# Kernel optimization log

Hardware: AMD Instinct MI355X
Metric: run time of the kernel (lower is better)

The kernel has to match this reference:

```python
import jax, jax.numpy as jnp
import numpy as np

EPS = 1e-7

def squash(t, axis=-1):
    sq = jnp.sum(jnp.square(t), axis=axis, keepdims=True)
    safe_norm = jnp.sqrt(sq + EPS)
    return t * (sq / (1.0 + sq)) / safe_norm


def setup_inputs() -> dict:
    key = jax.random.key(0)
    k1, k2 = jax.random.split(key)
    B, I, Din, N, D = 32, 1024, 32, 64, 32
    x = jax.random.normal(k1, (B, I, Din), dtype=jnp.float32)
    # glorot-ish scale ~ sqrt(2/(Din+D)) = 0.1767; use 0.1
    W = jax.random.normal(k2, (N, I, D, Din), dtype=jnp.float32) * 0.1
    return {"x": x, "W": W, "num_routing": 3}


def _infer(inputs_hat, logits):
    # softmax over the num_capsule axis (axis=1), matching tf.nn.softmax(logits, axis=1)
    route = jax.nn.softmax(logits, axis=1)                      # [B,N,1,I]
    routing = jnp.squeeze(jnp.matmul(route, inputs_hat), -2)    # [B,N,D]
    return squash(routing)


def reference(x, W, num_routing):
    # inputs_hat[b,n,i,d] = sum_k x[b,i,k] * W[n,i,d,k]
    inputs_hat = jnp.einsum('bik,nidk->bnid', x, W)             # [B,N,I,D]
    B, N, I, D = inputs_hat.shape
    ih_stop = jax.lax.stop_gradient(inputs_hat)
    logits = jnp.zeros((B, N, 1, I), dtype=inputs_hat.dtype)
    outputs = None
    for r in range(num_routing):
        if r == num_routing - 1:
            outputs = _infer(inputs_hat, logits)
        else:
            outputs = _infer(ih_stop, logits)
            # distances[b,n,1,i] = <outputs[b,n,:], ih_stop[b,n,i,:]>
            dist = jnp.matmul(outputs[:, :, None, :], jnp.swapaxes(ih_stop, -1, -2))
            logits = logits + dist
    return outputs
```

## Files before the change

### kernel.cpp

```cpp
#include <hip/hip_runtime.h>
#include <stdint.h>

#define II 1024
#define BBc 32
#define NN 64
#define DD 32
#define NDT 2048

typedef _Float16 half8 __attribute__((ext_vector_type(8)));
typedef float f32x4 __attribute__((ext_vector_type(4)));

__device__ __forceinline__ half8 ld_cvt8(const float* __restrict__ p) {
  const float4 v0 = *(const float4*)p;
  const float4 v1 = *(const float4*)(p + 4);
  half8 h;
  h[0] = (_Float16)v0.x; h[1] = (_Float16)v0.y; h[2] = (_Float16)v0.z; h[3] = (_Float16)v0.w;
  h[4] = (_Float16)v1.x; h[5] = (_Float16)v1.y; h[6] = (_Float16)v1.z; h[7] = (_Float16)v1.w;
  return h;
}

__global__ __launch_bounds__(256) void k1_mfma(
    const float* __restrict__ x, const float* __restrict__ W,
    _Float16* __restrict__ ih)
{
  __shared__ _Float16 lbuf[4][32][64];
  const int t = threadIdx.x;
  const int i = blockIdx.x;
  const int half_ = blockIdx.y;
  const int w = t >> 6;
  const int L = t & 63;
  const int lm = L & 15, q = L >> 4;

  half8 afrag[2];
#pragma unroll
  for (int mt = 0; mt < 2; ++mt)
    afrag[mt] = ld_cvt8(x + ((size_t)(mt * 16 + lm) * II + i) * 32 + q * 8);

  const int ndw = half_ * 1024 + w * 256;
  for (int g = 0; g < 4; ++g) {
#pragma unroll
    for (int nt = 0; nt < 4; ++nt) {
      const int nd = ndw + g * 64 + nt * 16 + lm;
      const int n = nd >> 5, d = nd & 31;
      const half8 bfrag = ld_cvt8(W + (size_t)n * (II * 1024) + (size_t)i * 1024 + d * 32 + q * 8);
      const f32x4 z = {0.f, 0.f, 0.f, 0.f};
      f32x4 acc0 = __builtin_amdgcn_mfma_f32_16x16x32_f16(afrag[0], bfrag, z, 0, 0, 0);
      f32x4 acc1 = __builtin_amdgcn_mfma_f32_16x16x32_f16(afrag[1], bfrag, z, 0, 0, 0);
#pragma unroll
      for (int r = 0; r < 4; ++r) {
        lbuf[w][q * 4 + r][nt * 16 + lm]      = (_Float16)acc0[r];
        lbuf[w][16 + q * 4 + r][nt * 16 + lm] = (_Float16)acc1[r];
      }
    }
    __syncthreads();
#pragma unroll
    for (int j = 0; j < 4; ++j) {
      const int row = j * 8 + (L >> 3);
      const int ndo = (L & 7) * 8;
      const half8 v = *(const half8*)&lbuf[w][row][ndo];
      *(half8*)(ih + ((size_t)row * II + i) * NDT + ndw + g * 64 + ndo) = v;
    }
    __syncthreads();
  }
}

__global__ __launch_bounds__(256) void s0red(
    const _Float16* __restrict__ ih, float* __restrict__ s0p)
{
  const int b = blockIdx.x, is = blockIdx.y;
  const int t = threadIdx.x;
  const _Float16* base = ih + ((size_t)b * II + is * 64) * NDT + t * 8;
  float a[8] = {};
#pragma unroll 8
  for (int ii = 0; ii < 64; ++ii) {
    const half8 v = *(const half8*)(base + (size_t)ii * NDT);
#pragma unroll
    for (int j = 0; j < 8; ++j) a[j] += (float)v[j];
  }
  float* o = s0p + ((size_t)is * BBc + b) * NDT + t * 8;
  *(float4*)(o + 0) = make_float4(a[0], a[1], a[2], a[3]);
  *(float4*)(o + 4) = make_float4(a[4], a[5], a[6], a[7]);
}

__global__ __launch_bounds__(256) void k3_route(
    const _Float16* __restrict__ ih, const float* __restrict__ o1,
    const float* __restrict__ o2, float* __restrict__ rpart)
{
  __shared__ float red[4][NN][DD + 1];
  const int t = threadIdx.x;
  const int b = blockIdx.x, it = blockIdx.y;
  const int w = t >> 6, lane = t & 63;
  float outr[DD];
  {
    const float4* p1 = (const float4*)(o1 + ((size_t)b * NN + lane) * DD);
    if (o2 != nullptr) {
      const float4* p2 = (const float4*)(o2 + ((size_t)b * NN + lane) * DD);
#pragma unroll
      for (int qq = 0; qq < 8; ++qq) {
        const float4 v1 = p1[qq], v2 = p2[qq];
        outr[qq * 4 + 0] = v1.x + v2.x; outr[qq * 4 + 1] = v1.y + v2.y;
        outr[qq * 4 + 2] = v1.z + v2.z; outr[qq * 4 + 3] = v1.w + v2.w;
      }
    } else {
#pragma unroll
      for (int qq = 0; qq < 8; ++qq) {
        const float4 v1 = p1[qq];
        outr[qq * 4 + 0] = v1.x; outr[qq * 4 + 1] = v1.y;
        outr[qq * 4 + 2] = v1.z; outr[qq * 4 + 3] = v1.w;
      }
    }
  }
  float racc[DD] = {};
  const _Float16* ibase = ih + (size_t)b * II * NDT + lane * DD;
  for (int jj = 0; jj < 8; ++jj) {
    const int i = it * 32 + w * 8 + jj;
    const half8* r8 = (const half8*)(ibase + (size_t)i * NDT);
    float ihr[DD];
#pragma unroll
    for (int qq = 0; qq < 4; ++qq) {
      const half8 v = r8[qq];
#pragma unroll
      for (int j = 0; j < 8; ++j) ihr[qq * 8 + j] = (float)v[j];
    }
    float dist = 0.f;
#pragma unroll
    for (int d = 0; d < DD; ++d) dist += outr[d] * ihr[d];
    float m = dist;
#pragma unroll
    for (int off = 32; off > 0; off >>= 1) m = fmaxf(m, __shfl_xor(m, off));
    const float e = __expf(dist - m);
    float ss = e;
#pragma unroll
    for (int off = 32; off > 0; off >>= 1) ss += __shfl_xor(ss, off);
    const float route = e / ss;
#pragma unroll
    for (int d = 0; d < DD; ++d) racc[d] += route * ihr[d];
  }
#pragma unroll
  for (int d = 0; d < DD; ++d) red[w][lane][d] = racc[d];
  __syncthreads();
  for (int j = t; j < NN * DD; j += 256) {
    const int n = j >> 5, d = j & 31;
    const float v = red[0][n][d] + red[1][n][d] + red[2][n][d] + red[3][n][d];
    rpart[((size_t)it * BBc + b) * NDT + n * DD + d] = v;
  }
}

__global__ __launch_bounds__(256) void k_rs(
    const float* __restrict__ parts, const int nparts, const float scale,
    float* __restrict__ dst)
{
  const int b = blockIdx.x;
  const int ng = blockIdx.y;
  const int t = threadIdx.x;
  const int n = ng * 8 + (t >> 5), d = t & 31;
  const size_t off = (size_t)b * NDT + n * DD + d;
  float s = 0.f;
  for (int c = 0; c < nparts; ++c) s += parts[(size_t)c * (BBc * NDT) + off];
  s *= scale;
  float sq = s * s;
#pragma unroll
  for (int m = 16; m > 0; m >>= 1) sq += __shfl_xor(sq, m);
  const float f = sq / ((1.f + sq) * sqrtf(sq + 1e-7f));
  dst[off] = s * f;
}

extern "C" void kernel_launch(void* const* d_in, const int* in_sizes, int n_in,
                              void* d_out, int out_size, void* d_ws, size_t ws_size,
                              hipStream_t stream) {
  (void)in_sizes; (void)n_in; (void)out_size; (void)ws_size;
  const float* x = (const float*)d_in[0];
  const float* W = (const float*)d_in[1];

  char* ws = (char*)d_ws;
  _Float16* ih = (_Float16*)ws;
  size_t off = (size_t)BBc * II * NDT * 2;
  float* s0p = (float*)(ws + off); off += (size_t)16 * BBc * NDT * 4;
  float* rpart = (float*)(ws + off); off += (size_t)32 * BBc * NDT * 4;
  float* outA = (float*)(ws + off); off += (size_t)BBc * NDT * 4;
  float* outB = (float*)(ws + off);
  float* outF = (float*)d_out;

  k1_mfma<<<dim3(II, 2), 256, 0, stream>>>(x, W, ih);
  s0red<<<dim3(BBc, 16), 256, 0, stream>>>(ih, s0p);
  k_rs<<<dim3(BBc, 8), 256, 0, stream>>>(s0p, 16, 1.f / 64.f, outA);
  k3_route<<<dim3(BBc, 32), 256, 0, stream>>>(ih, outA, nullptr, rpart);
  k_rs<<<dim3(BBc, 8), 256, 0, stream>>>(rpart, 32, 1.f, outB);
  k3_route<<<dim3(BBc, 32), 256, 0, stream>>>(ih, outA, outB, rpart);
  k_rs<<<dim3(BBc, 8), 256, 0, stream>>>(rpart, 32, 1.f, outF);
}
```

Baseline: 499.3 us.

## Fuse initial uniform-route sum into MFMA projection kernel, drop s0red pass

The projection kernel now computes partial sums over 8 input capsules per block while writing inputs_hat, storing fp16 partials. This removes the separate s0red kernel, which re-read the full inputs_hat tensor from memory. The block grid is reshaped to 128x8 with each warp looping over 8 i values, and the per-iteration __syncthreads are replaced with lgkmcnt waits because each warp uses only its own LDS slice. The costs are a larger partial buffer reduced in fp16 with 128 parts, and reliance on intra-warp LDS ordering being correct without barriers.

```diff
diff --git a/kernel.cpp b/kernel.cpp
--- a/kernel.cpp
+++ b/kernel.cpp
@@ -19,67 +19,67 @@
   return h;
 }
 
-__global__ __launch_bounds__(256) void k1_mfma(
+__global__ __launch_bounds__(256) void kA(
     const float* __restrict__ x, const float* __restrict__ W,
-    _Float16* __restrict__ ih)
+    _Float16* __restrict__ ih, _Float16* __restrict__ s0p)
 {
   __shared__ _Float16 lbuf[4][32][64];
   const int t = threadIdx.x;
-  const int i = blockIdx.x;
-  const int half_ = blockIdx.y;
+  const int ic = blockIdx.x;
+  const int ndc = blockIdx.y;
   const int w = t >> 6;
   const int L = t & 63;
   const int lm = L & 15, q = L >> 4;
+  const int ndw = ndc * 256 + w * 64;
 
-  half8 afrag[2];
-#pragma unroll
-  for (int mt = 0; mt < 2; ++mt)
-    afrag[mt] = ld_cvt8(x + ((size_t)(mt * 16 + lm) * II + i) * 32 + q * 8);
+  f32x4 s0acc[2][4] = {};
 
-  const int ndw = half_ * 1024 + w * 256;
-  for (int g = 0; g < 4; ++g) {
+  for (int ii = 0; ii < 8; ++ii) {
+    const int i = ic * 8 + ii;
+    half8 af0 = ld_cvt8(x + ((size_t)lm * II + i) * 32 + q * 8);
+    half8 af1 = ld_cvt8(x + ((size_t)(16 + lm) * II + i) * 32 + q * 8);
 #pragma unroll
     for (int nt = 0; nt < 4; ++nt) {
-      const int nd = ndw + g * 64 + nt * 16 + lm;
+      const int nd = ndw + nt * 16 + lm;
       const int n = nd >> 5, d = nd & 31;
-      const half8 bfrag = ld_cvt8(W + (size_t)n * (II * 1024) + (size_t)i * 1024 + d * 32 + q * 8);
+      const half8 bf = ld_cvt8(W + (size_t)n * (II * 1024) + (size_t)i * 1024 + d * 32 + q * 8);
       const f32x4 z = {0.f, 0.f, 0.f, 0.f};
-      f32x4 acc0 = __builtin_amdgcn_mfma_f32_16x16x32_f16(afrag[0], bfrag, z, 0, 0, 0);
-      f32x4 acc1 = __builtin_amdgcn_mfma_f32_16x16x32_f16(afrag[1], bfrag, z, 0, 0, 0);
+      f32x4 c0 = __builtin_amdgcn_mfma_f32_16x16x32_f16(af0, bf, z, 0, 0, 0);
+      f32x4 c1 = __builtin_amdgcn_mfma_f32_16x16x32_f16(af1, bf, z, 0, 0, 0);
+      s0acc[0][nt] += c0;
+      s0acc[1][nt] += c1;
 #pragma unroll
       for (int r = 0; r < 4; ++r) {
-        lbuf[w][q * 4 + r][nt * 16 + lm]      = (_Float16)acc0[r];
-        lbuf[w][16 + q * 4 + r][nt * 16 + lm] = (_Float16)acc1[r];
+        lbuf[w][q * 4 + r][nt * 16 + lm]      = (_Float16)c0[r];
+        lbuf[w][16 + q * 4 + r][nt * 16 + lm] = (_Float16)c1[r];
       }
     }
-    __syncthreads();
+    __asm__ volatile("s_waitcnt lgkmcnt(0)" ::: "memory");
 #pragma unroll
     for (int j = 0; j < 4; ++j) {
       const int row = j * 8 + (L >> 3);
       const int ndo = (L & 7) * 8;
       const half8 v = *(const half8*)&lbuf[w][row][ndo];
-      *(half8*)(ih + ((size_t)row * II + i) * NDT + ndw + g * 64 + ndo) = v;
+      *(half8*)(ih + ((size_t)row * II + i) * NDT + ndw + ndo) = v;
     }
-    __syncthreads();
+    __asm__ volatile("s_waitcnt lgkmcnt(0)" ::: "memory");
   }
-}
 
-__global__ __launch_bounds__(256) void s0red(
-    const _Float16* __restrict__ ih, float* __restrict__ s0p)
-{
-  const int b = blockIdx.x, is = blockIdx.y;
-  const int t = threadIdx.x;
-  const _Float16* base = ih + ((size_t)b * II + is * 64) * NDT + t * 8;
-  float a[8] = {};
-#pragma unroll 8
-  for (int ii = 0; ii < 64; ++ii) {
-    const half8 v = *(const half8*)(base + (size_t)ii * NDT);
 #pragma unroll
-    for (int j = 0; j < 8; ++j) a[j] += (float)v[j];
+  for (int nt = 0; nt < 4; ++nt)
+#pragma unroll
+    for (int r = 0; r < 4; ++r) {
+      lbuf[w][q * 4 + r][nt * 16 + lm]      = (_Float16)s0acc[0][nt][r];
+      lbuf[w][16 + q * 4 + r][nt * 16 + lm] = (_Float16)s0acc[1][nt][r];
+    }
+  __asm__ volatile("s_waitcnt lgkmcnt(0)" ::: "memory");
+#pragma unroll
+  for (int j = 0; j < 4; ++j) {
+    const int row = j * 8 + (L >> 3);
+    const int ndo = (L & 7) * 8;
+    const half8 v = *(const half8*)&lbuf[w][row][ndo];
+    *(half8*)(s0p + ((size_t)ic * BBc + row) * NDT + ndw + ndo) = v;
   }
-  float* o = s0p + ((size_t)is * BBc + b) * NDT + t * 8;
-  *(float4*)(o + 0) = make_float4(a[0], a[1], a[2], a[3]);
-  *(float4*)(o + 4) = make_float4(a[4], a[5], a[6], a[7]);
 }
 
 __global__ __launch_bounds__(256) void k3_route(
@@ -146,8 +146,9 @@
   }
 }
 
+template <typename T>
 __global__ __launch_bounds__(256) void k_rs(
-    const float* __restrict__ parts, const int nparts, const float scale,
+    const T* __restrict__ parts, const int nparts, const float scale,
     float* __restrict__ dst)
 {
   const int b = blockIdx.x;
@@ -156,7 +157,7 @@
   const int n = ng * 8 + (t >> 5), d = t & 31;
   const size_t off = (size_t)b * NDT + n * DD + d;
   float s = 0.f;
-  for (int c = 0; c < nparts; ++c) s += parts[(size_t)c * (BBc * NDT) + off];
+  for (int c = 0; c < nparts; ++c) s += (float)parts[(size_t)c * (BBc * NDT) + off];
   s *= scale;
   float sq = s * s;
 #pragma unroll
@@ -175,17 +176,16 @@
   char* ws = (char*)d_ws;
   _Float16* ih = (_Float16*)ws;
   size_t off = (size_t)BBc * II * NDT * 2;
-  float* s0p = (float*)(ws + off); off += (size_t)16 * BBc * NDT * 4;
+  _Float16* s0p = (_Float16*)(ws + off); off += (size_t)128 * BBc * NDT * 2;
   float* rpart = (float*)(ws + off); off += (size_t)32 * BBc * NDT * 4;
   float* outA = (float*)(ws + off); off += (size_t)BBc * NDT * 4;
   float* outB = (float*)(ws + off);
   float* outF = (float*)d_out;
 
-  k1_mfma<<<dim3(II, 2), 256, 0, stream>>>(x, W, ih);
-  s0red<<<dim3(BBc, 16), 256, 0, stream>>>(ih, s0p);
-  k_rs<<<dim3(BBc, 8), 256, 0, stream>>>(s0p, 16, 1.f / 64.f, outA);
+  kA<<<dim3(128, 8), 256, 0, stream>>>(x, W, ih, s0p);
+  k_rs<_Float16><<<dim3(BBc, 8), 256, 0, stream>>>(s0p, 128, 1.f / 64.f, outA);
   k3_route<<<dim3(BBc, 32), 256, 0, stream>>>(ih, outA, nullptr, rpart);
-  k_rs<<<dim3(BBc, 8), 256, 0, stream>>>(rpart, 32, 1.f, outB);
+  k_rs<float><<<dim3(BBc, 8), 256, 0, stream>>>(rpart, 32, 1.f, outB);
   k3_route<<<dim3(BBc, 32), 256, 0, stream>>>(ih, outA, outB, rpart);
-  k_rs<<<dim3(BBc, 8), 256, 0, stream>>>(rpart, 32, 1.f, outF);
+  k_rs<float><<<dim3(BBc, 8), 256, 0, stream>>>(rpart, 32, 1.f, outF);
 }
```

Result: slower. 520.2 us (+4.2%).
